# Performance work log

Measured on AMD Instinct MI355X. Metric: run time of the kernel, lower is better.

The kernel has to match this reference:

```python
import jax, jax.numpy as jnp
import numpy as np

B_T = 32      # input capsule types
C_T = 32      # output capsule types
K = 3         # conv kernel
STRIDE = 2
H = 4         # pose matrix side
HH = H * H
ITERS = 3
EPS = 1e-10
LN_2PI = np.float32(np.log(2.0 * np.pi))


def setup_inputs() -> dict:
    key = jax.random.key(0)
    k1, k2, k3, k4, k5 = jax.random.split(key, 5)
    b, win = 16, 14
    poses = jax.random.normal(k1, (b, HH * B_T, win, win), dtype=jnp.float32)
    activations = jax.random.uniform(k2, (b, B_T, win, win), dtype=jnp.float32)
    W = jax.random.normal(k3, (B_T, K, K, C_T, H, H), dtype=jnp.float32)
    beta_v = jax.random.normal(k4, (1, C_T, 1, 1), dtype=jnp.float32)
    beta_a = jax.random.normal(k5, (1, C_T, 1), dtype=jnp.float32)
    lambda_ = jnp.float32(0.01)
    return {"lambda_": lambda_, "poses": poses, "activations": activations,
            "W": W, "beta_v": beta_v, "beta_a": beta_a}


def _em_routing(lambda_, a_in, V, beta_v, beta_a, b, Bkk, Cww, ww):
    sg = jax.lax.stop_gradient
    R = jnp.full((b, Bkk, Cww), 1.0 / C_T, dtype=V.dtype)
    a = mu = None
    for i in range(ITERS):
        R4 = (R * a_in)[..., None]                       # (b,Bkk,Cww,1)
        sum_R = R4.sum(1)                                # (b,Cww,1)
        mu = ((R4 * V).sum(1) / sum_R)[:, None]          # (b,1,Cww,hh)
        sigma_sq = ((R4 * (V - mu) ** 2).sum(1) / sum_R)[:, None]
        cost = (beta_v + jnp.log(jnp.sqrt(sigma_sq).reshape(b, C_T, ww, HH) + EPS)) \
               * sum_R.reshape(b, C_T, ww, 1)            # (b,C,ww,hh)
        a = jax.nn.sigmoid(lambda_ * (beta_a - cost.sum(-1)))  # (b,C,ww)
        a = a.reshape(b, Cww)
        if i != ITERS - 1:
            Vd, mud, ssd = sg(V), sg(mu), sg(sigma_sq)
            ln_p = -(Vd - mud) ** 2 / (2.0 * ssd) - jnp.log(jnp.sqrt(ssd)) - 0.5 * LN_2PI
            p = jnp.exp(ln_p)                            # (b,Bkk,Cww,hh)
            ap = sg(a)[:, None, :] * p.sum(-1)           # (b,Bkk,Cww)
            R = sg(ap / (ap.sum(2, keepdims=True) + EPS) + EPS)
    return a, mu


def _forward(lambda_, poses, activations, W, beta_v, beta_a):
    b, win = poses.shape[0], poses.shape[2]
    w = (win - K) // STRIDE + 1
    ww = w * w
    Bkk = K * K * B_T
    Cww = ww * C_T
    pose = poses.reshape(b, HH, B_T, win, win).transpose(0, 2, 3, 4, 1)
    # patch extraction indices: row ri[i, ki] = stride*i + ki
    ri = (STRIDE * np.arange(w))[:, None] + np.arange(K)  # (w, K)
    P = pose[:, :, ri]
    P = P[:, :, :, :, ri]         # (b,B,w_i,K_i,w_j,K_j,hh)
    # stack order in torch: dim=-1 index = j*w + i, patch dims (K_i,K_j,hh)
    patches = P.transpose(0, 1, 3, 5, 6, 4, 2).reshape(b, B_T, K, K, HH, ww)
    # faithful to torch .view (row-major reinterpretation mixing hh and ww)
    poses_r = patches.reshape(b, B_T, K, K, 1, w, w, H, H)
    W_hat = W[None, :, :, :, :, None, None, :, :]          # (1,B,K,K,C,1,1,h,h)
    votes = jnp.matmul(W_hat, poses_r)                     # (b,B,K,K,C,w,w,h,h)
    # activation patches, same (j*w+i) ordering
    A = activations[:, :, ri]
    A = A[:, :, :, :, ri]         # (b,B,w_i,K_i,w_j,K_j)
    act_p = A.transpose(0, 1, 3, 5, 4, 2).reshape(b, B_T, K, K, ww)
    a_ = jnp.broadcast_to(act_p.reshape(b, Bkk, 1, ww), (b, Bkk, C_T, ww)).reshape(b, Bkk, Cww)
    V = votes.reshape(b, Bkk, Cww, HH)
    a, mu = _em_routing(lambda_, a_, V, beta_v, beta_a, b, Bkk, Cww, ww)
    return mu.reshape(b, C_T, w, w, HH), a.reshape(b, C_T, w, w)


def reference(lambda_, poses, activations, W, beta_v, beta_a):
    return _forward(lambda_, poses, activations, W, beta_v, beta_a)
```

## Files before the change

### kernel.cpp

```cpp
#include <hip/hip_runtime.h>

#define EPS 1e-10f
#define HALF_LN2PI 0.91893853320467274f
#define LOG2E 1.4426950408889634f


__device__ __forceinline__ float fexp2(float x) {
    float r;
    asm("v_exp_f32 %0, %1" : "=v"(r) : "v"(x));
    return r;
}
__device__ __forceinline__ float qxor1_add(float x) {
    float r;
    asm("v_add_f32 %0, %1, %1 quad_perm:[1,0,3,2] row_mask:0xf bank_mask:0xf"
        : "=v"(r) : "v"(x));
    return r;
}
__device__ __forceinline__ float qxor2_add(float x) {
    float r;
    asm("v_add_f32 %0, %1, %1 quad_perm:[2,3,0,1] row_mask:0xf bank_mask:0xf"
        : "=v"(r) : "v"(x));
    return r;
}

template <int IT>
__global__ __launch_bounds__(128)
void m_pass(const float* __restrict__ poses, const float* __restrict__ acts,
            float* __restrict__ Ptg, float* __restrict__ actp,
            const float* __restrict__ W,
            const float* __restrict__ ap_buf, const float* __restrict__ denom_prev,
            float* __restrict__ Mpart)
{
    __shared__ __align__(16) float Pt_lds[1152];
    __shared__ float act_lds[72];
    __shared__ float invd_lds[72];
    __shared__ __align__(16) float red[1152];

    const int tid  = threadIdx.x;
    const int wave = tid >> 6, lane = tid & 63;
    const int cl   = lane >> 2;
    const int bid  = blockIdx.x;
    const int blk  = bid >> 2, iq = bid & 3;
    const int bb   = blk / 36, p = blk - bb * 36;
    const int i0   = iq * 72;
    const size_t pbase  = (size_t)blk * 4608;
    const size_t apbase = (size_t)blk * 9216;

    if (IT == 0) {
        const int base = (p / 6) * 96 + (p % 6) * 16;
        for (int e = tid; e < 1152; e += 128) {
            int il = e >> 4, j = e & 15;
            int i = i0 + il;
            int hc = j >> 2, m = j & 3;
            int f = base + m * 4 + hc;
            int h = f / 36, sp = f - h * 36;
            int y = sp / 6, x = sp - y * 6;
            int B = i / 9, kk = i - B * 9;
            int ki = kk / 3, kj = kk - ki * 3;
            float v = poses[(size_t)((bb * 512 + h * 32 + B) * 14 + 2 * x + ki) * 14 + 2 * y + kj];
            Pt_lds[e] = v;
            Ptg[pbase + (size_t)i0 * 16 + e] = v;
        }
        const int y = p / 6, x = p - y * 6;
        for (int e = tid; e < 72; e += 128) {
            int i = i0 + e;
            int B = i / 9, kk = i - B * 9;
            int ki = kk / 3, kj = kk - ki * 3;
            float v = acts[(size_t)((bb * 32 + B) * 14 + 2 * x + ki) * 14 + 2 * y + kj];
            act_lds[e] = v;
            actp[blk * 288 + i] = v;
        }
    } else {
        const float4* src = (const float4*)(Ptg + pbase + (size_t)i0 * 16);
        float4* dst = (float4*)Pt_lds;
        for (int e = tid; e < 288; e += 128) dst[e] = src[e];
        for (int e = tid; e < 72; e += 128) {
            act_lds[e]  = actp[blk * 288 + i0 + e];
            invd_lds[e] = 1.0f / (denom_prev[bb * 288 + i0 + e] + EPS);
        }
    }
    __syncthreads();

    float acc[18];
#pragma unroll
    for (int k = 0; k < 18; ++k) acc[k] = 0.f;

    const float* Wt  = W + (size_t)(i0 + wave * 36) * 512 + (lane << 2);
    const float* apc = ap_buf + apbase + (size_t)(i0 + wave * 36) * 32 + cl;

#pragma unroll 6
    for (int t = 0; t < 36; ++t) {
        const int il = wave * 36 + t;
        const float4 wva = *(const float4*)(Wt + (size_t)t * 512);
        const float4 wvb = *(const float4*)(Wt + (size_t)t * 512 + 256);
        float Ra, Rb;
        if (IT == 0) {
            Ra = 1.0f / 32.0f; Rb = 1.0f / 32.0f;
        } else {
            const float inv = invd_lds[il];
            Ra = fmaf(apc[(size_t)t * 32],      inv, EPS);
            Rb = fmaf(apc[(size_t)t * 32 + 16], inv, EPS);
        }
        const float a_in = act_lds[il];
        const float R4a = Ra * a_in, R4b = Rb * a_in;
        acc[16] += R4a; acc[17] += R4b;
#pragma unroll
        for (int hc = 0; hc < 4; ++hc) {
            const float4 pv = *(const float4*)&Pt_lds[il * 16 + hc * 4];
            float Va = wva.x * pv.x + wva.y * pv.y + wva.z * pv.z + wva.w * pv.w;
            float Vb = wvb.x * pv.x + wvb.y * pv.y + wvb.z * pv.z + wvb.w * pv.w;
            acc[hc]      = fmaf(R4a, Va, acc[hc]);
            acc[4 + hc]  = fmaf(R4a * Va, Va, acc[4 + hc]);
            acc[8 + hc]  = fmaf(R4b, Vb, acc[8 + hc]);
            acc[12 + hc] = fmaf(R4b * Vb, Vb, acc[12 + hc]);
        }
    }

    if (wave == 1) {
#pragma unroll
        for (int k = 0; k < 18; ++k) red[lane * 18 + k] = acc[k];
    }
    __syncthreads();
    if (wave == 0) {
        float* mp = Mpart + (size_t)bid * 1152;
#pragma unroll
        for (int k = 0; k < 18; ++k)
            mp[k * 64 + lane] = acc[k] + red[lane * 18 + k];
    }
}

template <int FINAL>
__global__ __launch_bounds__(64)
void f_pass(float* __restrict__ Mpart, const float* __restrict__ beta_v,
            const float* __restrict__ beta_a, const float* __restrict__ lambda_p,
            float* __restrict__ d_out, float* __restrict__ denom_zero)
{
    const int lane = threadIdx.x;
    const int cl = lane >> 2, hr = lane & 3;
    const int blk = blockIdx.x;
    const int bb = blk / 36, p = blk - bb * 36;
    float* mp = Mpart + (size_t)blk * 4608;

    if (!FINAL && lane < 8)
        denom_zero[blk * 8 + lane] = 0.0f;

    float s[18];
#pragma unroll
    for (int k = 0; k < 18; ++k)
        s[k] = mp[k * 64 + lane] + mp[1152 + k * 64 + lane]
             + mp[2304 + k * 64 + lane] + mp[3456 + k * 64 + lane];

    const float lam = lambda_p[0];
    float muv[8], n2v[8], hlv[8], av[2];
#pragma unroll
    for (int q = 0; q < 2; ++q) {
        const int c = cl + q * 16;
        const float sR = s[16 + q];
        float ls = 0.f;
#pragma unroll
        for (int hc = 0; hc < 4; ++hc) {
            const float S1 = s[q * 8 + hc];
            const float S2 = s[q * 8 + 4 + hc];
            const float mu = S1 / sR;
            float ss = S2 / sR - mu * mu;
            ss = fmaxf(ss, 1e-30f);
            muv[q * 4 + hc] = mu;
            n2v[q * 4 + hc] = (-0.5f / ss) * LOG2E;
            hlv[q * 4 + hc] = (-0.5f * __logf(ss) - HALF_LN2PI) * LOG2E;
            ls += __logf(sqrtf(ss) + EPS);
        }
        ls += __shfl_xor(ls, 1);
        ls += __shfl_xor(ls, 2);
        const float cost = sR * (16.0f * beta_v[c] + ls);
        av[q] = 1.0f / (1.0f + __expf(-lam * (beta_a[c] - cost)));
    }

    if (FINAL) {
#pragma unroll
        for (int q = 0; q < 2; ++q) {
            const int c = cl + q * 16;
#pragma unroll
            for (int hc = 0; hc < 4; ++hc)
                d_out[(size_t)bb * 18432 + (size_t)(c * 36 + p) * 16 + hr * 4 + hc] = muv[q * 4 + hc];
            if (hr == 0)
                d_out[294912 + (size_t)bb * 1152 + c * 36 + p] = av[q];
        }
    } else {
        asm volatile("s_waitcnt vmcnt(0)" ::: "memory");
#pragma unroll
        for (int q = 0; q < 2; ++q) {
#pragma unroll
            for (int hc = 0; hc < 4; ++hc) {
                const int ix = lane * 4 + q * 256 + hc;
                mp[ix]        = muv[q * 4 + hc];
                mp[512 + ix]  = n2v[q * 4 + hc];
                mp[1024 + ix] = hlv[q * 4 + hc];
            }
            if (hr == 0) mp[1536 + cl + q * 16] = av[q];
        }
    }
}

__global__ __launch_bounds__(128)
void e_pass(const float* __restrict__ Ptg, const float* __restrict__ Mpart,
            const float* __restrict__ W,
            float* __restrict__ ap_buf, float* __restrict__ denom_next)
{
    __shared__ __align__(16) float Pt_lds[1152];
    __shared__ __align__(16) float ap_lds[2304];

    const int tid  = threadIdx.x;
    const int wave = tid >> 6, lane = tid & 63;
    const int cl   = lane >> 2, hr = lane & 3;
    const int bid  = blockIdx.x;
    const int blk  = bid >> 2, iq = bid & 3;
    const int bb   = blk / 36;
    const int i0   = iq * 72;
    const size_t pbase  = (size_t)blk * 4608;
    const size_t apbase = (size_t)blk * 9216;

    {
        const float4* src = (const float4*)(Ptg + pbase + (size_t)i0 * 16);
        float4* dst = (float4*)Pt_lds;
        for (int e = tid; e < 288; e += 128) dst[e] = src[e];
    }

    const float* st = Mpart + (size_t)blk * 4608;
    __align__(16) float mua[4], mub[4], na[4], nb[4], ha[4], hb[4];
    *(float4*)mua = *(const float4*)&st[lane * 4];
    *(float4*)mub = *(const float4*)&st[lane * 4 + 256];
    *(float4*)na  = *(const float4*)&st[512 + lane * 4];
    *(float4*)nb  = *(const float4*)&st[512 + lane * 4 + 256];
    *(float4*)ha  = *(const float4*)&st[1024 + lane * 4];
    *(float4*)hb  = *(const float4*)&st[1024 + lane * 4 + 256];
    const float aca = st[1536 + cl], acb = st[1536 + cl + 16];
    __syncthreads();

    const float* Wt = W + (size_t)(i0 + wave * 36) * 512 + (lane << 2);

#pragma unroll 6
    for (int t = 0; t < 36; ++t) {
        const int il = wave * 36 + t;
        const float4 wva = *(const float4*)(Wt + (size_t)t * 512);
        const float4 wvb = *(const float4*)(Wt + (size_t)t * 512 + 256);
        float pea = 0.f, peb = 0.f;
#pragma unroll
        for (int hc = 0; hc < 4; ++hc) {
            const float4 pv = *(const float4*)&Pt_lds[il * 16 + hc * 4];
            float Va = wva.x * pv.x + wva.y * pv.y + wva.z * pv.z + wva.w * pv.w;
            float Vb = wvb.x * pv.x + wvb.y * pv.y + wvb.z * pv.z + wvb.w * pv.w;
            float da = Va - mua[hc];
            float db = Vb - mub[hc];
            pea += fexp2(fmaf(da * da, na[hc], ha[hc]));
            peb += fexp2(fmaf(db * db, nb[hc], hb[hc]));
        }
        pea = qxor1_add(pea);
        pea = qxor2_add(pea);
        peb = qxor1_add(peb);
        peb = qxor2_add(peb);
        if (hr == 0) {
            ap_lds[il * 32 + cl]      = aca * pea;
            ap_lds[il * 32 + cl + 16] = acb * peb;
        }
    }
    __syncthreads();

    {
        const float4* s4 = (const float4*)ap_lds;
        float4* d4 = (float4*)(ap_buf + apbase + (size_t)i0 * 32);
        for (int e = tid; e < 576; e += 128) d4[e] = s4[e];
    }
    if (tid < 72) {
        float s = 0.f;
#pragma unroll
        for (int c = 0; c < 32; ++c)
            s += ap_lds[tid * 32 + ((c + tid) & 31)];
        atomicAdd(&denom_next[bb * 288 + i0 + tid], s);
    }
}

extern "C" void kernel_launch(void* const* d_in, const int* in_sizes, int n_in,
                              void* d_out, int out_size, void* d_ws, size_t ws_size,
                              hipStream_t stream)
{
    const float* lambda_p = (const float*)d_in[0];
    const float* poses    = (const float*)d_in[1];
    const float* acts     = (const float*)d_in[2];
    const float* W        = (const float*)d_in[3];
    const float* beta_v   = (const float*)d_in[4];
    const float* beta_a   = (const float*)d_in[5];
    float* out = (float*)d_out;

    float* ws     = (float*)d_ws;
    float* Ptg    = ws;
    float* actp   = Ptg + 2654208;
    float* ap_buf = actp + 165888;
    float* Mpart  = ap_buf + 5308416;
    float* denom0 = Mpart + 2654208;
    float* denom1 = denom0 + 4608;

    m_pass<0><<<2304, 128, 0, stream>>>(poses, acts, Ptg, actp, W, ap_buf, denom1, Mpart);
    f_pass<0><<<576, 64, 0, stream>>>(Mpart, beta_v, beta_a, lambda_p, out, denom0);
    e_pass<<<2304, 128, 0, stream>>>(Ptg, Mpart, W, ap_buf, denom0);
    m_pass<1><<<2304, 128, 0, stream>>>(poses, acts, Ptg, actp, W, ap_buf, denom0, Mpart);
    f_pass<0><<<576, 64, 0, stream>>>(Mpart, beta_v, beta_a, lambda_p, out, denom1);
    e_pass<<<2304, 128, 0, stream>>>(Ptg, Mpart, W, ap_buf, denom1);
    m_pass<2><<<2304, 128, 0, stream>>>(poses, acts, Ptg, actp, W, ap_buf, denom1, Mpart);
    f_pass<1><<<576, 64, 0, stream>>>(Mpart, beta_v, beta_a, lambda_p, out, denom0);
}
```

Measured before the change: 176.3 us.

## Fuse routing statistics pass into E-step kernel and drop f_pass launches

Removes the separate f_pass kernel between M and E steps: e_pass now reduces the four Mpart partial sums and computes mu, variance terms and activations itself, and m_pass zeroes the next denominator buffer. A small out_pass writes final outputs. This cuts two kernel launches and the write/read round trip of statistics, at the cost of redundant statistic computation in every e_pass block.

Measured after the change: 181.0 us. 1.03x slower.

```diff
diff --git a/kernel.cpp b/kernel.cpp
--- a/kernel.cpp
+++ b/kernel.cpp
@@ -29,7 +29,7 @@
             float* __restrict__ Ptg, float* __restrict__ actp,
             const float* __restrict__ W,
             const float* __restrict__ ap_buf, const float* __restrict__ denom_prev,
-            float* __restrict__ Mpart)
+            float* __restrict__ Mpart, float* __restrict__ denom_zero)
 {
     __shared__ __align__(16) float Pt_lds[1152];
     __shared__ float act_lds[72];
@@ -45,6 +45,9 @@
     const int i0   = iq * 72;
     const size_t pbase  = (size_t)blk * 4608;
     const size_t apbase = (size_t)blk * 9216;
+
+    if (tid < 72)
+        denom_zero[bb * 288 + i0 + tid] = 0.0f;
 
     if (IT == 0) {
         const int base = (p / 6) * 96 + (p % 6) * 16;
@@ -129,81 +132,10 @@
     }
 }
 
-template <int FINAL>
-__global__ __launch_bounds__(64)
-void f_pass(float* __restrict__ Mpart, const float* __restrict__ beta_v,
-            const float* __restrict__ beta_a, const float* __restrict__ lambda_p,
-            float* __restrict__ d_out, float* __restrict__ denom_zero)
-{
-    const int lane = threadIdx.x;
-    const int cl = lane >> 2, hr = lane & 3;
-    const int blk = blockIdx.x;
-    const int bb = blk / 36, p = blk - bb * 36;
-    float* mp = Mpart + (size_t)blk * 4608;
-
-    if (!FINAL && lane < 8)
-        denom_zero[blk * 8 + lane] = 0.0f;
-
-    float s[18];
-#pragma unroll
-    for (int k = 0; k < 18; ++k)
-        s[k] = mp[k * 64 + lane] + mp[1152 + k * 64 + lane]
-             + mp[2304 + k * 64 + lane] + mp[3456 + k * 64 + lane];
-
-    const float lam = lambda_p[0];
-    float muv[8], n2v[8], hlv[8], av[2];
-#pragma unroll
-    for (int q = 0; q < 2; ++q) {
-        const int c = cl + q * 16;
-        const float sR = s[16 + q];
-        float ls = 0.f;
-#pragma unroll
-        for (int hc = 0; hc < 4; ++hc) {
-            const float S1 = s[q * 8 + hc];
-            const float S2 = s[q * 8 + 4 + hc];
-            const float mu = S1 / sR;
-            float ss = S2 / sR - mu * mu;
-            ss = fmaxf(ss, 1e-30f);
-            muv[q * 4 + hc] = mu;
-            n2v[q * 4 + hc] = (-0.5f / ss) * LOG2E;
-            hlv[q * 4 + hc] = (-0.5f * __logf(ss) - HALF_LN2PI) * LOG2E;
-            ls += __logf(sqrtf(ss) + EPS);
-        }
-        ls += __shfl_xor(ls, 1);
-        ls += __shfl_xor(ls, 2);
-        const float cost = sR * (16.0f * beta_v[c] + ls);
-        av[q] = 1.0f / (1.0f + __expf(-lam * (beta_a[c] - cost)));
-    }
-
-    if (FINAL) {
-#pragma unroll
-        for (int q = 0; q < 2; ++q) {
-            const int c = cl + q * 16;
-#pragma unroll
-            for (int hc = 0; hc < 4; ++hc)
-                d_out[(size_t)bb * 18432 + (size_t)(c * 36 + p) * 16 + hr * 4 + hc] = muv[q * 4 + hc];
-            if (hr == 0)
-                d_out[294912 + (size_t)bb * 1152 + c * 36 + p] = av[q];
-        }
-    } else {
-        asm volatile("s_waitcnt vmcnt(0)" ::: "memory");
-#pragma unroll
-        for (int q = 0; q < 2; ++q) {
-#pragma unroll
-            for (int hc = 0; hc < 4; ++hc) {
-                const int ix = lane * 4 + q * 256 + hc;
-                mp[ix]        = muv[q * 4 + hc];
-                mp[512 + ix]  = n2v[q * 4 + hc];
-                mp[1024 + ix] = hlv[q * 4 + hc];
-            }
-            if (hr == 0) mp[1536 + cl + q * 16] = av[q];
-        }
-    }
-}
-
 __global__ __launch_bounds__(128)
 void e_pass(const float* __restrict__ Ptg, const float* __restrict__ Mpart,
-            const float* __restrict__ W,
+            const float* __restrict__ W, const float* __restrict__ beta_v,
+            const float* __restrict__ beta_a, const float* __restrict__ lambda_p,
             float* __restrict__ ap_buf, float* __restrict__ denom_next)
 {
     __shared__ __align__(16) float Pt_lds[1152];
@@ -225,15 +157,38 @@
         for (int e = tid; e < 288; e += 128) dst[e] = src[e];
     }
 
-    const float* st = Mpart + (size_t)blk * 4608;
     __align__(16) float mua[4], mub[4], na[4], nb[4], ha[4], hb[4];
-    *(float4*)mua = *(const float4*)&st[lane * 4];
-    *(float4*)mub = *(const float4*)&st[lane * 4 + 256];
-    *(float4*)na  = *(const float4*)&st[512 + lane * 4];
-    *(float4*)nb  = *(const float4*)&st[512 + lane * 4 + 256];
-    *(float4*)ha  = *(const float4*)&st[1024 + lane * 4];
-    *(float4*)hb  = *(const float4*)&st[1024 + lane * 4 + 256];
-    const float aca = st[1536 + cl], acb = st[1536 + cl + 16];
+    float aca, acb;
+    {
+        const float* mp = Mpart + (size_t)blk * 4608;
+        float s[18];
+#pragma unroll
+        for (int k = 0; k < 18; ++k)
+            s[k] = mp[k * 64 + lane] + mp[1152 + k * 64 + lane]
+                 + mp[2304 + k * 64 + lane] + mp[3456 + k * 64 + lane];
+        const float lam = lambda_p[0];
+#pragma unroll
+        for (int q = 0; q < 2; ++q) {
+            const int c = cl + q * 16;
+            const float sR = s[16 + q];
+            float ls = 0.f;
+#pragma unroll
+            for (int hc = 0; hc < 4; ++hc) {
+                const float mu = s[q * 8 + hc] / sR;
+                float ss = s[q * 8 + 4 + hc] / sR - mu * mu;
+                ss = fmaxf(ss, 1e-30f);
+                (q ? mub : mua)[hc] = mu;
+                (q ? nb : na)[hc] = (-0.5f / ss) * LOG2E;
+                (q ? hb : ha)[hc] = (-0.5f * __logf(ss) - HALF_LN2PI) * LOG2E;
+                ls += __logf(sqrtf(ss) + EPS);
+            }
+            ls += __shfl_xor(ls, 1);
+            ls += __shfl_xor(ls, 2);
+            const float cost = sR * (16.0f * beta_v[c] + ls);
+            const float av = 1.0f / (1.0f + __expf(-lam * (beta_a[c] - cost)));
+            if (q) acb = av; else aca = av;
+        }
+    }
     __syncthreads();
 
     const float* Wt = W + (size_t)(i0 + wave * 36) * 512 + (lane << 2);
@@ -276,6 +231,46 @@
         for (int c = 0; c < 32; ++c)
             s += ap_lds[tid * 32 + ((c + tid) & 31)];
         atomicAdd(&denom_next[bb * 288 + i0 + tid], s);
+    }
+}
+
+__global__ __launch_bounds__(64)
+void out_pass(const float* __restrict__ Mpart, const float* __restrict__ beta_v,
+              const float* __restrict__ beta_a, const float* __restrict__ lambda_p,
+              float* __restrict__ d_out)
+{
+    const int lane = threadIdx.x;
+    const int cl = lane >> 2, hr = lane & 3;
+    const int blk = blockIdx.x;
+    const int bb = blk / 36, p = blk - bb * 36;
+    const float* mp = Mpart + (size_t)blk * 4608;
+
+    float s[18];
+#pragma unroll
+    for (int k = 0; k < 18; ++k)
+        s[k] = mp[k * 64 + lane] + mp[1152 + k * 64 + lane]
+             + mp[2304 + k * 64 + lane] + mp[3456 + k * 64 + lane];
+
+    const float lam = lambda_p[0];
+#pragma unroll
+    for (int q = 0; q < 2; ++q) {
+        const int c = cl + q * 16;
+        const float sR = s[16 + q];
+        float ls = 0.f;
+#pragma unroll
+        for (int hc = 0; hc < 4; ++hc) {
+            const float mu = s[q * 8 + hc] / sR;
+            float ss = s[q * 8 + 4 + hc] / sR - mu * mu;
+            ss = fmaxf(ss, 1e-30f);
+            d_out[(size_t)bb * 18432 + (size_t)(c * 36 + p) * 16 + hr * 4 + hc] = mu;
+            ls += __logf(sqrtf(ss) + EPS);
+        }
+        ls += __shfl_xor(ls, 1);
+        ls += __shfl_xor(ls, 2);
+        const float cost = sR * (16.0f * beta_v[c] + ls);
+        const float av = 1.0f / (1.0f + __expf(-lam * (beta_a[c] - cost)));
+        if (hr == 0)
+            d_out[294912 + (size_t)bb * 1152 + c * 36 + p] = av;
     }
 }
 
@@ -299,12 +294,10 @@
     float* denom0 = Mpart + 2654208;
     float* denom1 = denom0 + 4608;
 
-    m_pass<0><<<2304, 128, 0, stream>>>(poses, acts, Ptg, actp, W, ap_buf, denom1, Mpart);
-    f_pass<0><<<576, 64, 0, stream>>>(Mpart, beta_v, beta_a, lambda_p, out, denom0);
-    e_pass<<<2304, 128, 0, stream>>>(Ptg, Mpart, W, ap_buf, denom0);
-    m_pass<1><<<2304, 128, 0, stream>>>(poses, acts, Ptg, actp, W, ap_buf, denom0, Mpart);
-    f_pass<0><<<576, 64, 0, stream>>>(Mpart, beta_v, beta_a, lambda_p, out, denom1);
-    e_pass<<<2304, 128, 0, stream>>>(Ptg, Mpart, W, ap_buf, denom1);
-    m_pass<2><<<2304, 128, 0, stream>>>(poses, acts, Ptg, actp, W, ap_buf, denom1, Mpart);
-    f_pass<1><<<576, 64, 0, stream>>>(Mpart, beta_v, beta_a, lambda_p, out, denom0);
-}
+    m_pass<0><<<2304, 128, 0, stream>>>(poses, acts, Ptg, actp, W, ap_buf, denom1, Mpart, denom0);
+    e_pass<<<2304, 128, 0, stream>>>(Ptg, Mpart, W, beta_v, beta_a, lambda_p, ap_buf, denom0);
+    m_pass<1><<<2304, 128, 0, stream>>>(poses, acts, Ptg, actp, W, ap_buf, denom0, Mpart, denom1);
+    e_pass<<<2304, 128, 0, stream>>>(Ptg, Mpart, W, beta_v, beta_a, lambda_p, ap_buf, denom1);
+    m_pass<1><<<2304, 128, 0, stream>>>(poses, acts, Ptg, actp, W, ap_buf, denom1, Mpart, denom0);
+    out_pass<<<576, 64, 0, stream>>>(Mpart, beta_v, beta_a, lambda_p, out);
+}
```
